# Performance work log

Measured on AMD Instinct MI355X. Metric: run time of the kernel, lower is better.

Reference implementation:

```python
import jax, jax.numpy as jnp
import numpy as np

EPS = 1e-6


def _normalize(A):
    # zero the diagonal, then symmetric degree normalization D @ A @ D.
    # D is diagonal with 1/(eps + sqrt(rowsum)), so D@A@D is an
    # elementwise row/column scale (same math, no NxN diag matmuls).
    N = A.shape[-1]
    A = A * (1.0 - jnp.eye(N, dtype=A.dtype))          # [B,N,N]
    d = 1.0 / (EPS + jnp.sqrt(jnp.sum(A, axis=2)))     # [B,N]
    return d[:, :, None] * A * d[:, None, :]           # [B,N,N]


def setup_inputs() -> dict:
    key = jax.random.key(0)
    k1, k2, k3, k4 = jax.random.split(key, 4)
    B, N, F, K, out_dim = 16, 2048, 64, 4, 128
    X = jax.random.uniform(k1, (B, N, F), dtype=jnp.float32)
    A = jax.random.uniform(k2, (B, N, N), dtype=jnp.float32)
    kernel = jax.random.normal(k3, (K * F, out_dim), dtype=jnp.float32) * 0.05
    bias = jax.random.normal(k4, (out_dim,), dtype=jnp.float32) * 0.05
    return {"X": X, "A": A, "kernel": kernel, "bias": bias}


def reference(X, A, kernel, bias):
    K = 4
    L = _normalize(A)                                  # [B,N,N]
    Xt = [X, jnp.matmul(L, X)]                         # T0, T1
    for k in range(2, K):
        Xt.append(2.0 * jnp.matmul(L, Xt[k - 1]) - Xt[k - 2])
    out = jnp.concatenate(Xt, axis=-1)                 # [B,N,K*F]
    out = jnp.matmul(out, kernel) + bias               # [B,N,out_dim]
    return jax.nn.relu(out)
```

## Files before the change

### kernel.cpp

```cpp
#include <hip/hip_runtime.h>

typedef __attribute__((ext_vector_type(4))) float  f32x4;
typedef __attribute__((ext_vector_type(8))) short  bf16x8;
typedef __attribute__((ext_vector_type(4))) int    i32x4;
typedef __attribute__((ext_vector_type(4))) unsigned short u16x4;

#define NB 16
#define NN 2048
#define FF 64

#define INV_SCALE (1.0f / (127.0f * 131072.0f))

__device__ __forceinline__ unsigned short f2bf(float x) {
  union { float f; unsigned int u; } c; c.f = x;
  unsigned int u = c.u;
  return (unsigned short)((u + 0x7fffu + ((u >> 16) & 1u)) >> 16);
}
__device__ __forceinline__ float bf2f(unsigned short b) {
  union { unsigned int u; float f; } c; c.u = (unsigned int)b << 16;
  return c.f;
}
__device__ __forceinline__ unsigned int fbits(float x) {
  union { float f; unsigned int u; } c; c.f = x; return c.u;
}

__device__ __forceinline__ void gload16(const void* g, void* l) {
  __builtin_amdgcn_global_load_lds(
      (const __attribute__((address_space(1))) void*)g,
      (__attribute__((address_space(3))) void*)l, 16, 0, 0);
}

#define BAR() asm volatile("s_barrier" ::: "memory")

__global__ __launch_bounds__(256) void rowsum_conv_kernel(
    const float* __restrict__ A, char* __restrict__ A8,
    float* __restrict__ dvec) {
  int row = blockIdx.x * 4 + (threadIdx.x >> 6);
  int lane = threadIdx.x & 63;
  int i = row & (NN - 1);
  const float* arow = A + (size_t)row * NN;
  char* orow = A8 + (size_t)row * NN;
  float diagval = __builtin_nontemporal_load(arow + i);
  float s = 0.f;
#pragma unroll
  for (int p = 0; p < 8; ++p) {
    int base = p * 256 + lane * 4;
    f32x4 v = __builtin_nontemporal_load((const f32x4*)(arow + base));
    s += v[0] + v[1] + v[2] + v[3];
    float y0 = fmaf(v[0], 127.f, 8388608.f);
    float y1 = fmaf(v[1], 127.f, 8388608.f);
    float y2 = fmaf(v[2], 127.f, 8388608.f);
    float y3 = fmaf(v[3], 127.f, 8388608.f);
    unsigned p01 = __builtin_amdgcn_perm(fbits(y1), fbits(y0), 0x0C0C0400u);
    unsigned p23 = __builtin_amdgcn_perm(fbits(y3), fbits(y2), 0x0C0C0400u);
    *(unsigned int*)(orow + base) =
        __builtin_amdgcn_perm(p23, p01, 0x05040100u);
  }
#pragma unroll
  for (int off = 32; off > 0; off >>= 1) s += __shfl_down(s, off, 64);
  asm volatile("s_waitcnt vmcnt(0)" ::: "memory");
  if (lane == 0) {
    orow[i] = 0;
    dvec[row] = 1.0f / (1e-6f + sqrtf(s - diagval));
  }
}

__global__ __launch_bounds__(256) void scale_transpose_kernel(
    const float* __restrict__ V, const float* __restrict__ dvec,
    char* __restrict__ Uh, char* __restrict__ Ul,
    unsigned short* __restrict__ Tb,
    const float* __restrict__ Kr, unsigned short* __restrict__ WT) {
  int bid = blockIdx.x;
  int tid = threadIdx.x;
  if (bid >= 512) {
    int idx = (bid - 512) * 256 + tid;
    int k = idx >> 7, c = idx & 127;
    WT[c * 256 + k] = f2bf(Kr[idx]);
    return;
  }
  int b = bid >> 5;
  int n0 = (bid & 31) * 64;
  __shared__ float t[64][65];
#pragma unroll
  for (int it = 0; it < 4; ++it) {
    int e = it * 256 + tid;
    int nl = e >> 4;
    int f0 = (e & 15) * 4;
    int n = n0 + nl;
    f32x4 v = *(const f32x4*)&V[((size_t)b * NN + n) * FF + f0];
    float dd = dvec[b * NN + n];
    u16x4 o;
#pragma unroll
    for (int j = 0; j < 4; ++j) { o[j] = f2bf(v[j]); t[f0 + j][nl] = v[j] * dd; }
    *(u16x4*)&Tb[((size_t)b * NN + n) * FF + f0] = o;
  }
  __syncthreads();
#pragma unroll
  for (int it = 0; it < 2; ++it) {
    int c = it * 256 + tid;
    int f = c >> 3, nl0 = (c & 7) * 8;
    unsigned long long ph = 0, pl = 0;
#pragma unroll
    for (int j = 0; j < 8; ++j) {
      int q = (int)rintf(t[f][nl0 + j] * 131072.f);
      q = q > 16383 ? 16383 : (q < -16383 ? -16383 : q);
      ph |= (unsigned long long)((unsigned int)(q >> 7) & 255u) << (8 * j);
      pl |= (unsigned long long)((unsigned int)(q & 127)) << (8 * j);
    }
    size_t o = ((size_t)b * FF + f) * NN + n0 + nl0;
    *(unsigned long long*)&Uh[o] = ph;
    *(unsigned long long*)&Ul[o] = pl;
  }
}

__global__ __launch_bounds__(256) void cheb_mm_kernel(
    const char* __restrict__ A8,
    const char* __restrict__ Uh,
    const char* __restrict__ Ul,
    const float* __restrict__ dvec,
    const unsigned short* __restrict__ prevb,
    unsigned short* __restrict__ Tbout,
    char* __restrict__ Uhout,
    char* __restrict__ Ulout,
    float cs) {
  __shared__ char lds[36864];
  int bid = blockIdx.x;
  int slot = bid >> 3;
  int b = (bid & 7) * 2 + (slot >> 5);
  int tm = slot & 31;
  int tid = threadIdx.x;
  int lane = tid & 63;
  int w = tid >> 6;
  int wm = w >> 1, wn = w & 1;
  int lr = lane >> 2;
  int gs = (lane & 3) ^ (lr & 3);
  int r16 = lane & 15, kq = lane >> 4;
  const int NT = NN / 64;

  const size_t abase = ((size_t)b * NN + (size_t)tm * 64) * NN;
  const size_t ubase = (size_t)b * FF * NN;

  i32x4 ach[2][2] = {};
  i32x4 acl[2][2] = {};

  auto stage = [&](int s, int kt) {
    int k0 = kt * 64;
    int r = w * 16 + lr;
    gload16(A8 + abase + (size_t)r * NN + k0 + gs * 16,
            &lds[s * 4096 + w * 1024]);
    gload16(Uh + ubase + (size_t)r * NN + k0 + gs * 16,
            &lds[12288 + s * 4096 + w * 1024]);
    gload16(Ul + ubase + (size_t)r * NN + k0 + gs * 16,
            &lds[24576 + s * 4096 + w * 1024]);
  };

  stage(0, 0); stage(1, 1); stage(2, 2);
  int s = 0;
  for (int t = 0; t < NT; ++t) {
    if (t < NT - 2)       asm volatile("s_waitcnt vmcnt(6)" ::: "memory");
    else if (t == NT - 2) asm volatile("s_waitcnt vmcnt(3)" ::: "memory");
    else                  asm volatile("s_waitcnt vmcnt(0)" ::: "memory");
    BAR();
    i32x4 af[2], uhf[2], ulf[2];
#pragma unroll
    for (int mi = 0; mi < 2; ++mi) {
      int row = wm * 32 + mi * 16 + r16;
      af[mi] = *(const i32x4*)&lds[s * 4096 + row * 64 + ((kq ^ (row & 3)) * 16)];
    }
#pragma unroll
    for (int ni = 0; ni < 2; ++ni) {
      int fr = wn * 32 + ni * 16 + r16;
      uhf[ni] = *(const i32x4*)&lds[12288 + s * 4096 + fr * 64 + ((kq ^ (fr & 3)) * 16)];
      ulf[ni] = *(const i32x4*)&lds[24576 + s * 4096 + fr * 64 + ((kq ^ (fr & 3)) * 16)];
    }
#pragma unroll
    for (int mi = 0; mi < 2; ++mi)
#pragma unroll
      for (int ni = 0; ni < 2; ++ni) {
        ach[mi][ni] = __builtin_amdgcn_mfma_i32_16x16x64_i8(
            af[mi], uhf[ni], ach[mi][ni], 0, 0, 0);
        acl[mi][ni] = __builtin_amdgcn_mfma_i32_16x16x64_i8(
            af[mi], ulf[ni], acl[mi][ni], 0, 0, 0);
      }
    BAR();
    if (t + 3 < NT) stage(s, t + 3);
    s = (s == 2) ? 0 : s + 1;
  }

  char (*th)[72]  = (char(*)[72])lds;
  char (*tlo)[72] = (char(*)[72])&lds[12288];
  int n0 = tm * 64;
#pragma unroll
  for (int mi = 0; mi < 2; ++mi) {
#pragma unroll
    for (int r = 0; r < 4; ++r) {
      int rl = wm * 32 + mi * 16 + kq * 4 + r;
      int row = n0 + rl;
      float dd = dvec[b * NN + row];
      float dcs = dd * cs;
#pragma unroll
      for (int ni = 0; ni < 2; ++ni) {
        int col = wn * 32 + ni * 16 + r16;
        size_t idx = ((size_t)b * NN + row) * FF + col;
        float c = 128.f * (float)ach[mi][ni][r] + (float)acl[mi][ni][r];
        float v = dcs * c;
        if (prevb) v -= bf2f(prevb[idx]);
        Tbout[idx] = f2bf(v);
        if (Uhout) {
          int q = (int)rintf(dd * v * 131072.f);
          q = q > 16383 ? 16383 : (q < -16383 ? -16383 : q);
          th[col][rl]  = (char)(q >> 7);
          tlo[col][rl] = (char)(q & 127);
        }
      }
    }
  }
  if (Uhout) {
    __syncthreads();
#pragma unroll
    for (int it = 0; it < 2; ++it) {
      int c = tid + it * 256;
      int f = c >> 3, nl0 = (c & 7) * 8;
      unsigned long long vh = *(const unsigned long long*)&th[f][nl0];
      unsigned long long vl = *(const unsigned long long*)&tlo[f][nl0];
      size_t o = ((size_t)b * FF + f) * NN + n0 + nl0;
      *(unsigned long long*)&Uhout[o] = vh;
      *(unsigned long long*)&Ulout[o] = vl;
    }
  }
}

__global__ __launch_bounds__(256) void final_gemm_kernel(
    const unsigned short* __restrict__ Tb,
    const unsigned short* __restrict__ WT,
    const float* __restrict__ bias,
    float* __restrict__ out) {
  __shared__ unsigned short lds[36864];
  const int M = NB * NN;
  int m0 = blockIdx.x * 64;
  int tid = threadIdx.x;
  int lane = tid & 63, w = tid >> 6;
  int wm = w >> 1, wn = w & 1;
  int lr = lane >> 3, gs = (lane & 7) ^ lr;
  int r16 = lane & 15, kq = lane >> 4;

  f32x4 acc[2][4] = {};

  auto stage = [&](int s, int kt) {
    const unsigned short* asrc = Tb + (size_t)kt * M * FF;
#pragma unroll
    for (int i = 0; i < 2; ++i) {
      int chunk = w * 2 + i;
      int r = chunk * 8 + lr;
      gload16(asrc + (size_t)(m0 + r) * FF + gs * 8,
              &lds[s * 4096 + chunk * 512]);
    }
#pragma unroll
    for (int i = 0; i < 4; ++i) {
      int chunk = w * 4 + i;
      int c = chunk * 8 + lr;
      gload16(WT + c * 256 + kt * 64 + gs * 8,
              &lds[12288 + s * 8192 + chunk * 512]);
    }
  };

  stage(0, 0); stage(1, 1); stage(2, 2);
  int s = 0;
  for (int t = 0; t < 4; ++t) {
    if (t < 2)       asm volatile("s_waitcnt vmcnt(12)" ::: "memory");
    else if (t == 2) asm volatile("s_waitcnt vmcnt(6)" ::: "memory");
    else             asm volatile("s_waitcnt vmcnt(0)" ::: "memory");
    BAR();
    bf16x8 af[2][2], bfr[4][2];
#pragma unroll
    for (int ks = 0; ks < 2; ++ks) {
#pragma unroll
      for (int mi = 0; mi < 2; ++mi) {
        int row = wm * 32 + mi * 16 + r16;
        af[mi][ks] = *(const bf16x8*)&lds[s * 4096 + row * 64 +
                                          (((ks * 4 + kq) ^ (row & 7)) * 8)];
      }
#pragma unroll
      for (int ni = 0; ni < 4; ++ni) {
        int fr = wn * 64 + ni * 16 + r16;
        bfr[ni][ks] = *(const bf16x8*)&lds[12288 + s * 8192 + fr * 64 +
                                           (((ks * 4 + kq) ^ (fr & 7)) * 8)];
      }
    }
#pragma unroll
    for (int ks = 0; ks < 2; ++ks)
#pragma unroll
      for (int mi = 0; mi < 2; ++mi)
#pragma unroll
        for (int ni = 0; ni < 4; ++ni)
          acc[mi][ni] = __builtin_amdgcn_mfma_f32_16x16x32_bf16(
              af[mi][ks], bfr[ni][ks], acc[mi][ni], 0, 0, 0);
    BAR();
    if (t + 3 < 4) stage(s, t + 3);
    s = (s == 2) ? 0 : s + 1;
  }

#pragma unroll
  for (int mi = 0; mi < 2; ++mi) {
#pragma unroll
    for (int r = 0; r < 4; ++r) {
      int row = m0 + wm * 32 + mi * 16 + kq * 4 + r;
#pragma unroll
      for (int ni = 0; ni < 4; ++ni) {
        int col = wn * 64 + ni * 16 + r16;
        float v = acc[mi][ni][r] + bias[col];
        out[(size_t)row * 128 + col] = v > 0.f ? v : 0.f;
      }
    }
  }
}

extern "C" void kernel_launch(void* const* d_in, const int* in_sizes, int n_in,
                              void* d_out, int out_size, void* d_ws, size_t ws_size,
                              hipStream_t stream) {
  const float* X    = (const float*)d_in[0];
  const float* A    = (const float*)d_in[1];
  const float* Kr   = (const float*)d_in[2];
  const float* bias = (const float*)d_in[3];
  float* out = (float*)d_out;
  char* ws = (char*)d_ws;

  const size_t SZ_A8 = (size_t)NB * NN * NN;
  const size_t SZ_D  = (size_t)NB * NN * 4;
  const size_t SZ_U  = (size_t)NB * FF * NN;
  const size_t SZ_TB = (size_t)NB * NN * FF * 2;
  const size_t TBE   = (size_t)NB * NN * FF;

  char*           A8  = ws;
  float*          dv  = (float*)(ws + SZ_A8);
  char*           Uha = ws + SZ_A8 + SZ_D;
  char*           Ula = Uha + SZ_U;
  char*           Uhb = Ula + SZ_U;
  char*           Ulb = Uhb + SZ_U;
  unsigned short* Tb  = (unsigned short*)(Ulb + SZ_U);
  unsigned short* WT  = (unsigned short*)(Ulb + SZ_U + 4 * SZ_TB);

  rowsum_conv_kernel<<<NB * NN / 4, 256, 0, stream>>>(A, A8, dv);
  scale_transpose_kernel<<<640, 256, 0, stream>>>(X, dv, Uha, Ula, Tb, Kr, WT);
  cheb_mm_kernel<<<512, 256, 0, stream>>>(A8, Uha, Ula, dv, nullptr,
                                          Tb + TBE, Uhb, Ulb, 1.0f * INV_SCALE);
  cheb_mm_kernel<<<512, 256, 0, stream>>>(A8, Uhb, Ulb, dv, Tb,
                                          Tb + 2 * TBE, Uha, Ula, 2.0f * INV_SCALE);
  cheb_mm_kernel<<<512, 256, 0, stream>>>(A8, Uha, Ula, dv, Tb + TBE,
                                          Tb + 3 * TBE, nullptr, nullptr, 2.0f * INV_SCALE);
  final_gemm_kernel<<<512, 256, 0, stream>>>(Tb, WT, bias, out);
}
```

Baseline: 137.7 us.

## Restructure cheb_mm to 512 threads with 128-wide K tiles and split A/U pipelines

The Chebyshev matmul kernel now runs 8 waves per block over the same 64x64 output tile, so each wave owns a 16x32 sub-tile instead of 32x32. The K step doubles to 128 bytes, and A uses a triple-buffered stage while the Uh/Ul operands use a separate double-buffered stage, with the LDS swizzle widened to 8 groups. The aim is to hide global-load latency better through more waves and fewer barrier iterations. In exchange, LDS use grows to 56 KB per block, which may lower block occupancy, and each wave does less MFMA work per LDS fragment load.

```diff
diff --git a/kernel.cpp b/kernel.cpp
--- a/kernel.cpp
+++ b/kernel.cpp
@@ -113,7 +113,7 @@
   }
 }
 
-__global__ __launch_bounds__(256) void cheb_mm_kernel(
+__global__ __launch_bounds__(512) void cheb_mm_kernel(
     const char* __restrict__ A8,
     const char* __restrict__ Uh,
     const char* __restrict__ Ul,
@@ -123,7 +123,7 @@
     char* __restrict__ Uhout,
     char* __restrict__ Ulout,
     float cs) {
-  __shared__ char lds[36864];
+  __shared__ char lds[57344];
   int bid = blockIdx.x;
   int slot = bid >> 3;
   int b = (bid & 7) * 2 + (slot >> 5);
@@ -132,101 +132,93 @@
   int lane = tid & 63;
   int w = tid >> 6;
   int wm = w >> 1, wn = w & 1;
-  int lr = lane >> 2;
-  int gs = (lane & 3) ^ (lr & 3);
+  int lr = lane >> 3;
+  int gs = (lane & 7) ^ lr;
   int r16 = lane & 15, kq = lane >> 4;
-  const int NT = NN / 64;
+  const int NT = NN / 128;
 
   const size_t abase = ((size_t)b * NN + (size_t)tm * 64) * NN;
   const size_t ubase = (size_t)b * FF * NN;
 
-  i32x4 ach[2][2] = {};
-  i32x4 acl[2][2] = {};
-
-  auto stage = [&](int s, int kt) {
-    int k0 = kt * 64;
-    int r = w * 16 + lr;
+  i32x4 ach[2] = {};
+  i32x4 acl[2] = {};
+
+  int r = w * 8 + lr;
+  auto stageU = [&](int su, int kt) {
+    int k0 = kt * 128;
+    gload16(Uh + ubase + (size_t)r * NN + k0 + gs * 16,
+            &lds[24576 + su * 8192 + w * 1024]);
+    gload16(Ul + ubase + (size_t)r * NN + k0 + gs * 16,
+            &lds[40960 + su * 8192 + w * 1024]);
+  };
+  auto stageA = [&](int sa, int kt) {
+    int k0 = kt * 128;
     gload16(A8 + abase + (size_t)r * NN + k0 + gs * 16,
-            &lds[s * 4096 + w * 1024]);
-    gload16(Uh + ubase + (size_t)r * NN + k0 + gs * 16,
-            &lds[12288 + s * 4096 + w * 1024]);
-    gload16(Ul + ubase + (size_t)r * NN + k0 + gs * 16,
-            &lds[24576 + s * 4096 + w * 1024]);
+            &lds[sa * 8192 + w * 1024]);
   };
 
-  stage(0, 0); stage(1, 1); stage(2, 2);
-  int s = 0;
+  stageU(0, 0); stageA(0, 0);
+  stageU(1, 1); stageA(1, 1);
+  stageA(2, 2);
   for (int t = 0; t < NT; ++t) {
-    if (t < NT - 2)       asm volatile("s_waitcnt vmcnt(6)" ::: "memory");
+    int sa = t % 3, su = t & 1;
+    if (t < NT - 2)       asm volatile("s_waitcnt vmcnt(4)" ::: "memory");
     else if (t == NT - 2) asm volatile("s_waitcnt vmcnt(3)" ::: "memory");
     else                  asm volatile("s_waitcnt vmcnt(0)" ::: "memory");
     BAR();
-    i32x4 af[2], uhf[2], ulf[2];
-#pragma unroll
-    for (int mi = 0; mi < 2; ++mi) {
-      int row = wm * 32 + mi * 16 + r16;
-      af[mi] = *(const i32x4*)&lds[s * 4096 + row * 64 + ((kq ^ (row & 3)) * 16)];
-    }
+    int ar = wm * 16 + r16;
+#pragma unroll
+    for (int j = 0; j < 2; ++j) {
+      i32x4 af = *(const i32x4*)&lds[sa * 8192 + ar * 128 +
+                                     (((j * 4 + kq) ^ (ar & 7)) * 16)];
+#pragma unroll
+      for (int ni = 0; ni < 2; ++ni) {
+        int fr = wn * 32 + ni * 16 + r16;
+        int fo = fr * 128 + (((j * 4 + kq) ^ (fr & 7)) * 16);
+        i32x4 uhf = *(const i32x4*)&lds[24576 + su * 8192 + fo];
+        i32x4 ulf = *(const i32x4*)&lds[40960 + su * 8192 + fo];
+        ach[ni] = __builtin_amdgcn_mfma_i32_16x16x64_i8(af, uhf, ach[ni], 0, 0, 0);
+        acl[ni] = __builtin_amdgcn_mfma_i32_16x16x64_i8(af, ulf, acl[ni], 0, 0, 0);
+      }
+    }
+    BAR();
+    if (t + 2 < NT) stageU((t + 2) & 1, t + 2);
+    if (t + 3 < NT) stageA((t + 3) % 3, t + 3);
+  }
+
+  char (*th)[72]  = (char(*)[72])lds;
+  char (*tlo)[72] = (char(*)[72])&lds[8192];
+  int n0 = tm * 64;
+#pragma unroll
+  for (int rg = 0; rg < 4; ++rg) {
+    int rl = wm * 16 + kq * 4 + rg;
+    int row = n0 + rl;
+    float dd = dvec[b * NN + row];
+    float dcs = dd * cs;
 #pragma unroll
     for (int ni = 0; ni < 2; ++ni) {
-      int fr = wn * 32 + ni * 16 + r16;
-      uhf[ni] = *(const i32x4*)&lds[12288 + s * 4096 + fr * 64 + ((kq ^ (fr & 3)) * 16)];
-      ulf[ni] = *(const i32x4*)&lds[24576 + s * 4096 + fr * 64 + ((kq ^ (fr & 3)) * 16)];
-    }
-#pragma unroll
-    for (int mi = 0; mi < 2; ++mi)
-#pragma unroll
-      for (int ni = 0; ni < 2; ++ni) {
-        ach[mi][ni] = __builtin_amdgcn_mfma_i32_16x16x64_i8(
-            af[mi], uhf[ni], ach[mi][ni], 0, 0, 0);
-        acl[mi][ni] = __builtin_amdgcn_mfma_i32_16x16x64_i8(
-            af[mi], ulf[ni], acl[mi][ni], 0, 0, 0);
-      }
-    BAR();
-    if (t + 3 < NT) stage(s, t + 3);
-    s = (s == 2) ? 0 : s + 1;
-  }
-
-  char (*th)[72]  = (char(*)[72])lds;
-  char (*tlo)[72] = (char(*)[72])&lds[12288];
-  int n0 = tm * 64;
-#pragma unroll
-  for (int mi = 0; mi < 2; ++mi) {
-#pragma unroll
-    for (int r = 0; r < 4; ++r) {
-      int rl = wm * 32 + mi * 16 + kq * 4 + r;
-      int row = n0 + rl;
-      float dd = dvec[b * NN + row];
-      float dcs = dd * cs;
-#pragma unroll
-      for (int ni = 0; ni < 2; ++ni) {
-        int col = wn * 32 + ni * 16 + r16;
-        size_t idx = ((size_t)b * NN + row) * FF + col;
-        float c = 128.f * (float)ach[mi][ni][r] + (float)acl[mi][ni][r];
-        float v = dcs * c;
-        if (prevb) v -= bf2f(prevb[idx]);
-        Tbout[idx] = f2bf(v);
-        if (Uhout) {
-          int q = (int)rintf(dd * v * 131072.f);
-          q = q > 16383 ? 16383 : (q < -16383 ? -16383 : q);
-          th[col][rl]  = (char)(q >> 7);
-          tlo[col][rl] = (char)(q & 127);
-        }
+      int col = wn * 32 + ni * 16 + r16;
+      size_t idx = ((size_t)b * NN + row) * FF + col;
+      float c = 128.f * (float)ach[ni][rg] + (float)acl[ni][rg];
+      float v = dcs * c;
+      if (prevb) v -= bf2f(prevb[idx]);
+      Tbout[idx] = f2bf(v);
+      if (Uhout) {
+        int q = (int)rintf(dd * v * 131072.f);
+        q = q > 16383 ? 16383 : (q < -16383 ? -16383 : q);
+        th[col][rl]  = (char)(q >> 7);
+        tlo[col][rl] = (char)(q & 127);
       }
     }
   }
   if (Uhout) {
     __syncthreads();
-#pragma unroll
-    for (int it = 0; it < 2; ++it) {
-      int c = tid + it * 256;
-      int f = c >> 3, nl0 = (c & 7) * 8;
-      unsigned long long vh = *(const unsigned long long*)&th[f][nl0];
-      unsigned long long vl = *(const unsigned long long*)&tlo[f][nl0];
-      size_t o = ((size_t)b * FF + f) * NN + n0 + nl0;
-      *(unsigned long long*)&Uhout[o] = vh;
-      *(unsigned long long*)&Ulout[o] = vl;
-    }
+    int f = tid >> 3, nb = (tid & 7) * 8;
+    unsigned long long vh = *(const unsigned long long*)&th[f][nb];
+    unsigned long long vl = *(const unsigned long long*)&tlo[f][nb];
+    size_t o = ((size_t)b * FF + f) * NN + n0 + nb;
+    *(unsigned long long*)&Uhout[o] = vh;
+    *(unsigned long long*)&Ulout[o] = vl;
   }
 }
 
@@ -342,11 +334,11 @@
 
   rowsum_conv_kernel<<<NB * NN / 4, 256, 0, stream>>>(A, A8, dv);
   scale_transpose_kernel<<<640, 256, 0, stream>>>(X, dv, Uha, Ula, Tb, Kr, WT);
-  cheb_mm_kernel<<<512, 256, 0, stream>>>(A8, Uha, Ula, dv, nullptr,
+  cheb_mm_kernel<<<512, 512, 0, stream>>>(A8, Uha, Ula, dv, nullptr,
                                           Tb + TBE, Uhb, Ulb, 1.0f * INV_SCALE);
-  cheb_mm_kernel<<<512, 256, 0, stream>>>(A8, Uhb, Ulb, dv, Tb,
+  cheb_mm_kernel<<<512, 512, 0, stream>>>(A8, Uhb, Ulb, dv, Tb,
                                           Tb + 2 * TBE, Uha, Ula, 2.0f * INV_SCALE);
-  cheb_mm_kernel<<<512, 256, 0, stream>>>(A8, Uha, Ula, dv, Tb + TBE,
+  cheb_mm_kernel<<<512, 512, 0, stream>>>(A8, Uha, Ula, dv, Tb + TBE,
                                           Tb + 3 * TBE, nullptr, nullptr, 2.0f * INV_SCALE);
   final_gemm_kernel<<<512, 256, 0, stream>>>(Tb, WT, bias, out);
 }
```

After: 118.1 us. -14.2%, faster.
